# Kernel tuning notes

Hardware: AMD Instinct MI355X
Metric: run time of the kernel (lower is better)

## Reference

```python
import jax, jax.numpy as jnp
import numpy as np
from jax import lax

NUM_CLASSES = 10
NUM_ITER = 3
DN = ('NCHW', 'OIHW', 'NCHW')


def squash(t, axis=-1):
    sq = (t ** 2).sum(axis=axis, keepdims=True)
    return (sq / (1.0 + sq)) * t / jnp.sqrt(sq)


def setup_inputs() -> dict:
    key = jax.random.key(0)
    ks = jax.random.split(key, 12)
    B = 512
    s = 0.05  # param scale for numerical stability
    return {
        'x': jax.random.normal(ks[0], (B, 1, 28, 28), jnp.float32),
        'conv1_w': jax.random.normal(ks[1], (256, 1, 9, 9), jnp.float32) * s,
        'conv1_b': jax.random.normal(ks[2], (256,), jnp.float32) * s,
        'prim_w': jax.random.normal(ks[3], (8, 32, 256, 9, 9), jnp.float32) * s,
        'prim_b': jax.random.normal(ks[4], (8, 32), jnp.float32) * s,
        'route_w': jax.random.normal(ks[5], (NUM_CLASSES, 32 * 6 * 6, 8, 16), jnp.float32),
        'dec_w1': jax.random.normal(ks[6], (512, 16 * NUM_CLASSES), jnp.float32) * s,
        'dec_b1': jax.random.normal(ks[7], (512,), jnp.float32) * s,
        'dec_w2': jax.random.normal(ks[8], (1024, 512), jnp.float32) * s,
        'dec_b2': jax.random.normal(ks[9], (1024,), jnp.float32) * s,
        'dec_w3': jax.random.normal(ks[10], (784, 1024), jnp.float32) * s,
        'dec_b3': jax.random.normal(ks[11], (784,), jnp.float32) * s,
    }


def reference(x, conv1_w, conv1_b, prim_w, prim_b, route_w,
              dec_w1, dec_b1, dec_w2, dec_b2, dec_w3, dec_b3):
    B = x.shape[0]
    # conv1 + relu: [B,256,20,20]
    h = lax.conv_general_dilated(x, conv1_w, (1, 1), 'VALID', dimension_numbers=DN)
    h = jax.nn.relu(h + conv1_b[None, :, None, None])
    # primary capsules: 8 parallel convs fused into one conv with 8*32 out channels
    kw = prim_w.reshape(8 * 32, 256, 9, 9)
    u = lax.conv_general_dilated(h, kw, (2, 2), 'VALID', dimension_numbers=DN)
    u = u + prim_b.reshape(-1)[None, :, None, None]          # [B,256,6,6]
    u = u.reshape(B, 8, 32 * 6 * 6).transpose(0, 2, 1)       # [B,1152,8]
    u = squash(u, axis=-1)
    # digit capsules: priors [C,B,R,16]
    priors = jnp.einsum('bri,crio->cbro', u, route_w)
    logits = jnp.zeros_like(priors)
    for i in range(NUM_ITER):
        probs = jax.nn.softmax(logits, axis=2)
        v = squash((probs * priors).sum(axis=2, keepdims=True))  # [C,B,1,16]
        if i != NUM_ITER - 1:
            logits = logits + (priors * v).sum(axis=-1, keepdims=True)
    caps = v.squeeze(2).transpose(1, 0, 2)                    # [B,C,16]
    classes = jnp.sqrt((caps ** 2).sum(axis=-1))              # [B,C]
    classes = jax.nn.softmax(classes, axis=1)
    y = jax.nn.one_hot(jnp.argmax(classes, axis=1), NUM_CLASSES, dtype=caps.dtype)
    d = (caps * y[:, :, None]).reshape(B, -1)                 # [B,160]
    d = jax.nn.relu(d @ dec_w1.T + dec_b1)
    d = jax.nn.relu(d @ dec_w2.T + dec_b2)
    recon = jax.nn.sigmoid(d @ dec_w3.T + dec_b3)             # [B,784]
    return classes, recon
```

## Files before the change

### kernel.cpp

```cpp
#include <hip/hip_runtime.h>
#include <math.h>


typedef _Float16 f16;
typedef _Float16 f16x8 __attribute__((ext_vector_type(8)));
typedef _Float16 f16x4 __attribute__((ext_vector_type(4)));
typedef float f32x4 __attribute__((ext_vector_type(4)));

__device__ __forceinline__ void gl_lds16(const void* g, void* l) {
  __builtin_amdgcn_global_load_lds(
      (const __attribute__((address_space(1))) void*)g,
      (__attribute__((address_space(3))) void*)l, 16, 0, 0);
}

__global__ void im2col_kernel(const float* __restrict__ x, f16* __restrict__ A)
{
  const int c = blockIdx.x * 256 + threadIdx.x;
  const int m = c / 12, kc = c - m * 12;
  const int b = m / 400, rem = m - b * 400;
  const int oy = rem / 20, ox = rem - oy * 20;
  const float* xb = x + b * 784;
  f16x8 v;
#pragma unroll
  for (int j = 0; j < 8; ++j) {
    const int k = kc * 8 + j;
    float val = 0.f;
    if (k < 81) {
      const int ky = k / 9, kx = k - ky * 9;
      val = xb[(oy + ky) * 28 + ox + kx];
    }
    v[j] = (f16)val;
  }
  *(f16x8*)&A[(size_t)m * 96 + kc * 8] = v;
}

__global__ void c1trans_kernel(const float* __restrict__ w, f16* __restrict__ wt1)
{
  const int idx = blockIdx.x * 256 + threadIdx.x;
  const int oc = idx / 96, k = idx - oc * 96;
  wt1[idx] = (k < 81) ? (f16)w[oc * 81 + k] : (f16)0.f;
}

__global__ __launch_bounds__(256) void conv1_mfma_kernel(
    const f16* __restrict__ A, const f16* __restrict__ wt1,
    const float* __restrict__ bias, f16* __restrict__ ht)
{
  __shared__ f16 sm[8192];
  const int t = threadIdx.x;
  const int wv = t >> 6, lane = t & 63;
  const int id = blockIdx.x;
  const int mb = id >> 1, nb = id & 1;
  const int m0 = mb * 128, n0 = nb * 128;

  const int chunk = (lane & 3) ^ ((lane >> 3) & 3);
  long aoff[2], boff[2];
#pragma unroll
  for (int i = 0; i < 2; ++i) {
    const int r = wv * 32 + i * 16 + (lane >> 2);
    aoff[i] = (long)(m0 + r) * 192 + chunk * 16;
    boff[i] = (long)(n0 + r) * 192 + chunk * 16;
  }
  const char* ac = (const char*)A;
  const char* bc = (const char*)wt1;

  const int lrow = lane & 15, quad = lane >> 4;
  const int qx = quad ^ ((lrow >> 1) & 3);
  const int wm = wv & 1, wn = wv >> 1;
  f32x4 acc[4][4] = {};

  for (int s = 0; s < 3; ++s) {
    const long kstep = (long)s * 64;
    __syncthreads();
    {
      char* dA = (char*)sm + wv * 2048;
      char* dB = (char*)sm + 8192 + wv * 2048;
      gl_lds16(ac + aoff[0] + kstep, dA);
      gl_lds16(ac + aoff[1] + kstep, dA + 1024);
      gl_lds16(bc + boff[0] + kstep, dB);
      gl_lds16(bc + boff[1] + kstep, dB + 1024);
    }
    __syncthreads();
    const f16* As = sm;
    const f16* Bs = sm + 4096;
    f16x8 af[4], bf[4];
#pragma unroll
    for (int mt = 0; mt < 4; ++mt)
      af[mt] = *(const f16x8*)&As[(wm * 64 + mt * 16 + lrow) * 32 + qx * 8];
#pragma unroll
    for (int nt = 0; nt < 4; ++nt)
      bf[nt] = *(const f16x8*)&Bs[(wn * 64 + nt * 16 + lrow) * 32 + qx * 8];
#pragma unroll
    for (int mt = 0; mt < 4; ++mt)
#pragma unroll
      for (int nt = 0; nt < 4; ++nt)
        acc[mt][nt] = __builtin_amdgcn_mfma_f32_16x16x32_f16(
            af[mt], bf[nt], acc[mt][nt], 0, 0, 0);
  }

#pragma unroll
  for (int nt = 0; nt < 4; ++nt) {
    const int n = n0 + wn * 64 + nt * 16 + lrow;
    const float bv = bias[n];
#pragma unroll
    for (int mt = 0; mt < 4; ++mt) {
      const int mbase = m0 + wm * 64 + mt * 16 + quad * 4;
#pragma unroll
      for (int rg = 0; rg < 4; ++rg)
        ht[(size_t)(mbase + rg) * 256 + n] =
            (f16)fmaxf(acc[mt][nt][rg] + bv, 0.f);
    }
  }
}

__global__ __launch_bounds__(256) void wtrans_kernel(
    const float* __restrict__ w, f16* __restrict__ wt)
{
  __shared__ float tile[64 * 83];
  const int oc = blockIdx.x;
  const int icq = blockIdx.y;
  const int t = threadIdx.x;
  const float* src = w + (size_t)oc * 20736 + (size_t)icq * 64 * 81;
  for (int idx = t; idx < 5184; idx += 256) {
    const int ici = idx / 81, kk = idx - ici * 81;
    tile[ici * 83 + kk] = src[idx];
  }
  __syncthreads();
  f16* dst = wt + (size_t)oc * 20736 + icq * 64;
  for (int idx = t; idx < 5184; idx += 256) {
    const int kk = idx >> 6, ici = idx & 63;
    dst[kk * 256 + ici] = (f16)tile[ici * 83 + kk];
  }
}

__global__ __launch_bounds__(256) void prim_mfma_kernel(
    const f16* __restrict__ ht, const f16* __restrict__ wt,
    f16* __restrict__ part)
{
  __shared__ f16 sm[24576];
  const int t = threadIdx.x;
  const int wv = t >> 6, lane = t & 63;
  const int id = blockIdx.x;
  const int ks = (id >> 3) & 7;
  const int nb = (id >> 6) & 1;
  const int mb = (id & 7) + 8 * (id >> 7);
  const int m0 = mb * 128, n0 = nb * 128;

  const int chunk = (lane & 3) ^ ((lane >> 3) & 3);
  long aoff[2], boff[2];
#pragma unroll
  for (int i = 0; i < 2; ++i) {
    const int r = wv * 32 + i * 16 + (lane >> 2);
    const int m = m0 + r;
    const int b = m / 36, pos = m - b * 36;
    const int oy = pos / 6, ox = pos - oy * 6;
    aoff[i] = (long)(((b * 20 + 2 * oy) * 20 + 2 * ox) * 256) * 2 + chunk * 16;
    boff[i] = (long)(n0 + r) * 41472 + chunk * 16;
  }
  const char* htc = (const char*)ht;
  const char* wtc = (const char*)wt;

  const int lrow = lane & 15, quad = lane >> 4;
  const int qx = quad ^ ((lrow >> 1) & 3);
  const int wm = wv & 1, wn = wv >> 1;
  f32x4 acc[4][4] = {};

  const int s0 = ks * 81;

#define STAGE(S, BUFB)                                                        \
  {                                                                           \
    const int kykx = (S) >> 3, icb = (S) & 7;                                 \
    const int ky = kykx / 9, kx = kykx - ky * 9;                              \
    const long astep = (long)((((ky * 20 + kx) * 256) + icb * 32) * 2);       \
    const long bstep = (long)(((kykx * 256) + icb * 32) * 2);                 \
    char* dA = (char*)sm + (BUFB) + wv * 2048;                                \
    char* dB = (char*)sm + (BUFB) + 8192 + wv * 2048;                         \
    gl_lds16(htc + aoff[0] + astep, dA);                                      \
    gl_lds16(htc + aoff[1] + astep, dA + 1024);                               \
    gl_lds16(wtc + boff[0] + bstep, dB);                                      \
    gl_lds16(wtc + boff[1] + bstep, dB + 1024);                               \
  }

#define CONSUME(BUFI)                                                         \
  {                                                                           \
    const f16* As = sm + (BUFI);                                              \
    const f16* Bs = sm + (BUFI) + 4096;                                       \
    f16x8 af[4], bf[4];                                                       \
    _Pragma("unroll") for (int mt = 0; mt < 4; ++mt)                          \
        af[mt] = *(const f16x8*)&As[(wm * 64 + mt * 16 + lrow) * 32 + qx * 8];\
    _Pragma("unroll") for (int nt = 0; nt < 4; ++nt)                          \
        bf[nt] = *(const f16x8*)&Bs[(wn * 64 + nt * 16 + lrow) * 32 + qx * 8];\
    _Pragma("unroll") for (int mt = 0; mt < 4; ++mt)                          \
        _Pragma("unroll") for (int nt = 0; nt < 4; ++nt)                      \
            acc[mt][nt] = __builtin_amdgcn_mfma_f32_16x16x32_f16(             \
                af[mt], bf[nt], acc[mt][nt], 0, 0, 0);                        \
  }

  STAGE(s0, 0);
  STAGE(s0 + 1, 16384);
  int bS = 32768;
  int bC = 0;
  for (int K = 0; K < 79; ++K) {
    asm volatile("s_waitcnt vmcnt(4)" ::: "memory");
    __builtin_amdgcn_s_barrier();
    asm volatile("" ::: "memory");
    STAGE(s0 + K + 2, bS);
    __builtin_amdgcn_s_setprio(1);
    CONSUME(bC >> 1);
    __builtin_amdgcn_s_setprio(0);
    bS += 16384; if (bS == 49152) bS = 0;
    bC += 16384; if (bC == 49152) bC = 0;
  }
  asm volatile("s_waitcnt vmcnt(4)" ::: "memory");
  __builtin_amdgcn_s_barrier();
  asm volatile("" ::: "memory");
  __builtin_amdgcn_s_setprio(1);
  CONSUME(bC >> 1);
  __builtin_amdgcn_s_setprio(0);
  bC += 16384; if (bC == 49152) bC = 0;
  asm volatile("s_waitcnt vmcnt(0)" ::: "memory");
  __builtin_amdgcn_s_barrier();
  asm volatile("" ::: "memory");
  CONSUME(bC >> 1);
#undef STAGE
#undef CONSUME

  f16* pp = part + (size_t)ks * 4718592;
#pragma unroll
  for (int mt = 0; mt < 4; ++mt) {
    const int mbase = m0 + wm * 64 + mt * 16 + quad * 4;
#pragma unroll
    for (int nt = 0; nt < 4; ++nt) {
      const int n = n0 + wn * 64 + nt * 16 + lrow;
      const int np = (n & 31) * 8 + (n >> 5);
#pragma unroll
      for (int rg = 0; rg < 4; ++rg)
        pp[(size_t)(mbase + rg) * 256 + np] = (f16)acc[mt][nt][rg];
    }
  }
}

__global__ void squash_kernel(const f16* __restrict__ part,
                              const float* __restrict__ bias,
                              f16* __restrict__ u16)
{
  const int tid = blockIdx.x * 256 + threadIdx.x;
  if (tid >= 512 * 36 * 32) return;
  const int cc = tid & 31;
  const int row = tid >> 5;
  const int b = row / 36;
  const int pos = row - b * 36;
  const f16* p = part + (size_t)row * 256 + cc * 8;
  float v[8] = {};
#pragma unroll
  for (int ksl = 0; ksl < 8; ++ksl) {
    const f16x8 a = *(const f16x8*)(p + (size_t)ksl * 4718592);
#pragma unroll
    for (int i = 0; i < 8; ++i) v[i] += (float)a[i];
  }
  float sq = 0.f;
#pragma unroll
  for (int i = 0; i < 8; ++i) {
    v[i] += bias[i * 32 + cc];
    sq = fmaf(v[i], v[i], sq);
  }
  const float scale = sq / ((1.f + sq) * sqrtf(sq));
  f16x8 st;
#pragma unroll
  for (int i = 0; i < 8; ++i) st[i] = (f16)(v[i] * scale);
  *(f16x8*)&u16[(size_t)(b * 1152 + pos * 32 + cc) * 8] = st;
}

__global__ __launch_bounds__(256, 4) void priors_kernel(
    const f16* __restrict__ u16, const float* __restrict__ rw,
    f16* __restrict__ P)
{
  const int t = threadIdx.x;
  const int rl = t >> 2, oq = t & 3;
  const int rs = blockIdx.x * 64 + rl;
  const int pos = rs >> 5, cc = rs & 31;
  const int r_true = cc * 36 + pos;
  const int b0 = blockIdx.y * 64;
  const int c = blockIdx.z;

  float4 wreg[8];
  const float* wbase = rw + (size_t)(c * 1152 + r_true) * 128 + oq * 4;
#pragma unroll
  for (int k = 0; k < 8; ++k)
    wreg[k] = *(const float4*)(wbase + k * 16);

  f16* pbase = P + (size_t)((c * 512 + b0) * 1152 + rs) * 16 + oq * 4;
  const f16* ubase = u16 + (size_t)(b0 * 1152 + rs) * 8;

  for (int b = 0; b < 64; ++b) {
    const f16x8 uv = *(const f16x8*)(ubase + (size_t)b * 9216);
    float ax = 0.f, ay = 0.f, az = 0.f, aw = 0.f;
#pragma unroll
    for (int k = 0; k < 8; ++k) {
      const float uk = (float)uv[k];
      ax = fmaf(uk, wreg[k].x, ax);
      ay = fmaf(uk, wreg[k].y, ay);
      az = fmaf(uk, wreg[k].z, az);
      aw = fmaf(uk, wreg[k].w, aw);
    }
    f16x4 st;
    st[0] = (f16)ax; st[1] = (f16)ay; st[2] = (f16)az; st[3] = (f16)aw;
    *(f16x4*)(pbase + (size_t)b * 18432) = st;
  }
}

__device__ __forceinline__ float wave_sum(float v) {
#pragma unroll
  for (int off = 32; off > 0; off >>= 1) v += __shfl_xor(v, off);
  return v;
}
__device__ __forceinline__ float wave_max(float v) {
#pragma unroll
  for (int off = 32; off > 0; off >>= 1) v = fmaxf(v, __shfl_xor(v, off));
  return v;
}

__global__ __launch_bounds__(256, 2) void routing_kernel(
    const f16* __restrict__ Pg, float* __restrict__ caps)
{
  const int c = blockIdx.x >> 9;
  const int b = blockIdx.x & 511;
  const int t = threadIdx.x;
  const int wid = t >> 6;
  const int lane = t & 63;
  __shared__ float xred[4 * 17];

  float P[5][16];
  float lg[5];
  const int nk = (t < 128) ? 5 : 4;
#pragma unroll
  for (int k = 0; k < 5; ++k)
#pragma unroll
    for (int o = 0; o < 16; ++o) P[k][o] = 0.f;

  const f16* pbase = Pg + (size_t)((c * 512 + b) * 1152) * 16;
#pragma unroll
  for (int k = 0; k < 5; ++k) {
    if (k < nk) {
      const int r = t + (k << 8);
      const f16x8 p0 = *(const f16x8*)&pbase[(size_t)r * 16];
      const f16x8 p1 = *(const f16x8*)&pbase[(size_t)r * 16 + 8];
#pragma unroll
      for (int o = 0; o < 8; ++o) {
        P[k][o]     = (float)p0[o];
        P[k][o + 8] = (float)p1[o];
      }
    }
  }

  float v[16];
  {
    float sq = 0.f;
#pragma unroll
    for (int o = 0; o < 16; ++o) {
      float p = 0.f;
#pragma unroll
      for (int k = 0; k < 5; ++k) p += P[k][o];
      p = wave_sum(p);
      if (lane == 0) xred[wid * 17 + o] = p;
      v[o] = 0.f;
    }
    __syncthreads();
#pragma unroll
    for (int o = 0; o < 16; ++o) {
      const float s = (xred[o] + xred[17 + o] + xred[34 + o] + xred[51 + o]) *
                      (1.f / 1152.f);
      v[o] = s;
      sq = fmaf(s, s, sq);
    }
    const float scale = sq / ((1.f + sq) * sqrtf(sq));
#pragma unroll
    for (int o = 0; o < 16; ++o) v[o] *= scale;
    __syncthreads();
  }
#pragma unroll
  for (int k = 0; k < 5; ++k) {
    float a = 0.f;
#pragma unroll
    for (int o = 0; o < 16; ++o) a = fmaf(P[k][o], v[o], a);
    lg[k] = a;
  }

  for (int it = 1; it < 3; ++it) {
    float m = -1e30f;
#pragma unroll
    for (int k = 0; k < 5; ++k) if (k < nk) m = fmaxf(m, lg[k]);
    m = wave_max(m);
    if (lane == 0) xred[wid * 17 + 16] = m;
    __syncthreads();
    const float mx = fmaxf(fmaxf(xred[16], xred[17 + 16]),
                           fmaxf(xred[34 + 16], xred[51 + 16]));
    __syncthreads();
    float e[5];
#pragma unroll
    for (int k = 0; k < 5; ++k) e[k] = (k < nk) ? expf(lg[k] - mx) : 0.f;
    float pS = 0.f;
#pragma unroll
    for (int k = 0; k < 5; ++k) pS += e[k];
    pS = wave_sum(pS);
    if (lane == 0) xred[wid * 17 + 16] = pS;
#pragma unroll
    for (int o = 0; o < 16; ++o) {
      float p = 0.f;
#pragma unroll
      for (int k = 0; k < 5; ++k) p = fmaf(e[k], P[k][o], p);
      p = wave_sum(p);
      if (lane == 0) xred[wid * 17 + o] = p;
    }
    __syncthreads();
    const float S = xred[16] + xred[17 + 16] + xred[34 + 16] + xred[51 + 16];
    const float inv = 1.f / S;
    float sq = 0.f;
#pragma unroll
    for (int o = 0; o < 16; ++o) {
      const float s = (xred[o] + xred[17 + o] + xred[34 + o] + xred[51 + o]) * inv;
      v[o] = s;
      sq = fmaf(s, s, sq);
    }
    const float scale = sq / ((1.f + sq) * sqrtf(sq));
#pragma unroll
    for (int o = 0; o < 16; ++o) v[o] *= scale;
    __syncthreads();
    if (it < 2) {
#pragma unroll
      for (int k = 0; k < 5; ++k) {
        float a = 0.f;
#pragma unroll
        for (int o = 0; o < 16; ++o) a = fmaf(P[k][o], v[o], a);
        lg[k] += a;
      }
    }
  }
  if (t == 0) {
    float* cp = &caps[(b * 10 + c) * 16];
#pragma unroll
    for (int o = 0; o < 16; ++o) cp[o] = v[o];
  }
}

__global__ void classes_kernel(const float* __restrict__ caps,
                               float* __restrict__ out_classes,
                               float* __restrict__ d0)
{
  const int b = blockIdx.x * 256 + threadIdx.x;
  if (b >= 512) return;
  float nrm[10];
#pragma unroll
  for (int cc = 0; cc < 10; ++cc) {
    float sq = 0.f;
#pragma unroll
    for (int o = 0; o < 16; ++o) {
      const float vv = caps[(b * 10 + cc) * 16 + o];
      sq = fmaf(vv, vv, sq);
    }
    nrm[cc] = sqrtf(sq);
  }
  float mx = nrm[0]; int cs = 0;
#pragma unroll
  for (int cc = 1; cc < 10; ++cc)
    if (nrm[cc] > mx) { mx = nrm[cc]; cs = cc; }
  float e[10], ssum = 0.f;
#pragma unroll
  for (int cc = 0; cc < 10; ++cc) { e[cc] = expf(nrm[cc] - mx); ssum += e[cc]; }
  const float inv = 1.f / ssum;
#pragma unroll
  for (int cc = 0; cc < 10; ++cc) out_classes[b * 10 + cc] = e[cc] * inv;
#pragma unroll
  for (int cc = 0; cc < 10; ++cc)
#pragma unroll
    for (int o = 0; o < 16; ++o)
      d0[b * 160 + cc * 16 + o] = (cc == cs) ? caps[(b * 10 + cc) * 16 + o] : 0.f;
}

__global__ __launch_bounds__(256, 2) void fc_kernel(
    const float* __restrict__ A, const float* __restrict__ W,
    const float* __restrict__ bias, float* __restrict__ C,
    int N, int K, int act)
{
  __shared__ float As[64][17];
  __shared__ float Ws[64][17];
  const int t = threadIdx.x;
  const int tm = t >> 4, tn = t & 15;
  const int m0 = blockIdx.y << 6, n0 = blockIdx.x << 6;
  const int lr = t >> 2, lq = (t & 3) << 2;
  float acc[4][4] = {};
  for (int k0 = 0; k0 < K; k0 += 16) {
    const float4 av = *(const float4*)&A[(m0 + lr) * K + k0 + lq];
    float4 wv = make_float4(0.f, 0.f, 0.f, 0.f);
    const int wn = n0 + lr;
    if (wn < N) wv = *(const float4*)&W[wn * K + k0 + lq];
    __syncthreads();
    As[lr][lq+0] = av.x; As[lr][lq+1] = av.y; As[lr][lq+2] = av.z; As[lr][lq+3] = av.w;
    Ws[lr][lq+0] = wv.x; Ws[lr][lq+1] = wv.y; Ws[lr][lq+2] = wv.z; Ws[lr][lq+3] = wv.w;
    __syncthreads();
#pragma unroll
    for (int kk = 0; kk < 16; ++kk) {
      float a[4], w[4];
#pragma unroll
      for (int i = 0; i < 4; ++i) a[i] = As[tm * 4 + i][kk];
#pragma unroll
      for (int j = 0; j < 4; ++j) w[j] = Ws[tn * 4 + j][kk];
#pragma unroll
      for (int i = 0; i < 4; ++i)
#pragma unroll
        for (int j = 0; j < 4; ++j) acc[i][j] = fmaf(a[i], w[j], acc[i][j]);
    }
  }
#pragma unroll
  for (int i = 0; i < 4; ++i) {
    const int m = m0 + tm * 4 + i;
#pragma unroll
    for (int j = 0; j < 4; ++j) {
      const int n = n0 + tn * 4 + j;
      if (n < N) {
        float vv = acc[i][j] + bias[n];
        vv = act ? (1.f / (1.f + expf(-vv))) : fmaxf(vv, 0.f);
        C[m * N + n] = vv;
      }
    }
  }
}

extern "C" void kernel_launch(void* const* d_in, const int* in_sizes, int n_in,
                              void* d_out, int out_size, void* d_ws, size_t ws_size,
                              hipStream_t stream)
{
  const float* x       = (const float*)d_in[0];
  const float* conv1_w = (const float*)d_in[1];
  const float* conv1_b = (const float*)d_in[2];
  const float* prim_w  = (const float*)d_in[3];
  const float* prim_b  = (const float*)d_in[4];
  const float* route_w = (const float*)d_in[5];
  const float* dec_w1  = (const float*)d_in[6];
  const float* dec_b1  = (const float*)d_in[7];
  const float* dec_w2  = (const float*)d_in[8];
  const float* dec_b2  = (const float*)d_in[9];
  const float* dec_w3  = (const float*)d_in[10];
  const float* dec_b3  = (const float*)d_in[11];
  float* out = (float*)d_out;

  char* ws = (char*)d_ws;
  f16*   ht   = (f16*)(ws);
  f16*   wtp  = (f16*)(ws + 104857600);
  f16*   part = (f16*)(ws + 115474432);
  f16*   A16  = (f16*)(ws + 115474432);
  f16*   wt1  = (f16*)(ws + 190971904);
  f16*   u16  = (f16*)(ws + 191021056);
  f16*   P    = (f16*)(ws);
  float* caps = (float*)(ws + 200458240);
  float* d0   = (float*)(ws + 200785920);
  float* d1   = (float*)(ws + 201113600);
  float* d2   = (float*)(ws + 202162176);

  hipLaunchKernelGGL(im2col_kernel, dim3(9600), dim3(256), 0, stream, x, A16);
  hipLaunchKernelGGL(c1trans_kernel, dim3(96), dim3(256), 0, stream,
                     conv1_w, wt1);
  hipLaunchKernelGGL(conv1_mfma_kernel, dim3(3200), dim3(256), 0, stream,
                     A16, wt1, conv1_b, ht);
  hipLaunchKernelGGL(wtrans_kernel, dim3(256, 4), dim3(256), 0, stream,
                     prim_w, wtp);
  hipLaunchKernelGGL(prim_mfma_kernel, dim3(2304), dim3(256), 0, stream,
                     ht, wtp, part);
  hipLaunchKernelGGL(squash_kernel, dim3(2304), dim3(256), 0, stream,
                     part, prim_b, u16);
  hipLaunchKernelGGL(priors_kernel, dim3(18, 8, 10), dim3(256), 0, stream,
                     u16, route_w, P);
  hipLaunchKernelGGL(routing_kernel, dim3(5120), dim3(256), 0, stream,
                     P, caps);
  hipLaunchKernelGGL(classes_kernel, dim3(2), dim3(256), 0, stream,
                     caps, out, d0);
  hipLaunchKernelGGL(fc_kernel, dim3(8, 8), dim3(256), 0, stream,
                     d0, dec_w1, dec_b1, d1, 512, 160, 0);
  hipLaunchKernelGGL(fc_kernel, dim3(16, 8), dim3(256), 0, stream,
                     d1, dec_w2, dec_b2, d2, 1024, 512, 0);
  hipLaunchKernelGGL(fc_kernel, dim3(13, 8), dim3(256), 0, stream,
                     d2, dec_w3, dec_b3, out + 5120, 784, 1024, 1);
}
```

Measured before the change: 750.7 us.

## Fuse priors computation into routing kernel, drop materialized priors tensor

Removes the separate priors kernel that wrote a large f16 priors tensor to global memory. Each routing block now recomputes its priors from the squashed capsules and a pre-converted f16 copy of the routing weights, which a new small prep kernel produces in the capsule order used by routing. This avoids a large write and re-read of intermediate data, at the cost of extra FMAs, more registers and per-thread strided weight reads that rely on cache reuse across batch blocks.

```diff
diff --git a/kernel.cpp b/kernel.cpp
--- a/kernel.cpp
+++ b/kernel.cpp
@@ -270,42 +270,15 @@
   *(f16x8*)&u16[(size_t)(b * 1152 + pos * 32 + cc) * 8] = st;
 }
 
-__global__ __launch_bounds__(256, 4) void priors_kernel(
-    const f16* __restrict__ u16, const float* __restrict__ rw,
-    f16* __restrict__ P)
-{
-  const int t = threadIdx.x;
-  const int rl = t >> 2, oq = t & 3;
-  const int rs = blockIdx.x * 64 + rl;
+__global__ void rwprep_kernel(const float* __restrict__ rw, f16* __restrict__ rwh)
+{
+  const int rs = blockIdx.x;
+  const int c  = blockIdx.y;
+  const int t  = threadIdx.x;
   const int pos = rs >> 5, cc = rs & 31;
   const int r_true = cc * 36 + pos;
-  const int b0 = blockIdx.y * 64;
-  const int c = blockIdx.z;
-
-  float4 wreg[8];
-  const float* wbase = rw + (size_t)(c * 1152 + r_true) * 128 + oq * 4;
-#pragma unroll
-  for (int k = 0; k < 8; ++k)
-    wreg[k] = *(const float4*)(wbase + k * 16);
-
-  f16* pbase = P + (size_t)((c * 512 + b0) * 1152 + rs) * 16 + oq * 4;
-  const f16* ubase = u16 + (size_t)(b0 * 1152 + rs) * 8;
-
-  for (int b = 0; b < 64; ++b) {
-    const f16x8 uv = *(const f16x8*)(ubase + (size_t)b * 9216);
-    float ax = 0.f, ay = 0.f, az = 0.f, aw = 0.f;
-#pragma unroll
-    for (int k = 0; k < 8; ++k) {
-      const float uk = (float)uv[k];
-      ax = fmaf(uk, wreg[k].x, ax);
-      ay = fmaf(uk, wreg[k].y, ay);
-      az = fmaf(uk, wreg[k].z, az);
-      aw = fmaf(uk, wreg[k].w, aw);
-    }
-    f16x4 st;
-    st[0] = (f16)ax; st[1] = (f16)ay; st[2] = (f16)az; st[3] = (f16)aw;
-    *(f16x4*)(pbase + (size_t)b * 18432) = st;
-  }
+  const float v = rw[(size_t)(c * 1152 + r_true) * 128 + t];
+  rwh[(size_t)(c * 1152 + rs) * 128 + t] = (f16)v;
 }
 
 __device__ __forceinline__ float wave_sum(float v) {
@@ -320,7 +293,8 @@
 }
 
 __global__ __launch_bounds__(256, 2) void routing_kernel(
-    const f16* __restrict__ Pg, float* __restrict__ caps)
+    const f16* __restrict__ u16, const f16* __restrict__ rwh,
+    float* __restrict__ caps)
 {
   const int c = blockIdx.x >> 9;
   const int b = blockIdx.x & 511;
@@ -337,17 +311,26 @@
 #pragma unroll
     for (int o = 0; o < 16; ++o) P[k][o] = 0.f;
 
-  const f16* pbase = Pg + (size_t)((c * 512 + b) * 1152) * 16;
+  const f16* ub = u16 + (size_t)b * 9216;
+  const f16* wb = rwh + (size_t)c * 147456;
 #pragma unroll
   for (int k = 0; k < 5; ++k) {
     if (k < nk) {
-      const int r = t + (k << 8);
-      const f16x8 p0 = *(const f16x8*)&pbase[(size_t)r * 16];
-      const f16x8 p1 = *(const f16x8*)&pbase[(size_t)r * 16 + 8];
-#pragma unroll
-      for (int o = 0; o < 8; ++o) {
-        P[k][o]     = (float)p0[o];
-        P[k][o + 8] = (float)p1[o];
+      const int rs = t + (k << 8);
+      const f16x8 uv = *(const f16x8*)&ub[(size_t)rs * 8];
+      float uf[8];
+#pragma unroll
+      for (int i = 0; i < 8; ++i) uf[i] = (float)uv[i];
+      const f16* wr = wb + (size_t)rs * 128;
+#pragma unroll
+      for (int kk = 0; kk < 8; ++kk) {
+        const f16x8 w0 = *(const f16x8*)&wr[kk * 16];
+        const f16x8 w1 = *(const f16x8*)&wr[kk * 16 + 8];
+#pragma unroll
+        for (int o = 0; o < 8; ++o) {
+          P[k][o]     = fmaf(uf[kk], (float)w0[o], P[k][o]);
+          P[k][o + 8] = fmaf(uf[kk], (float)w1[o], P[k][o + 8]);
+        }
       }
     }
   }
@@ -550,7 +533,7 @@
   f16*   A16  = (f16*)(ws + 115474432);
   f16*   wt1  = (f16*)(ws + 190971904);
   f16*   u16  = (f16*)(ws + 191021056);
-  f16*   P    = (f16*)(ws);
+  f16*   rwh  = (f16*)(ws);
   float* caps = (float*)(ws + 200458240);
   float* d0   = (float*)(ws + 200785920);
   float* d1   = (float*)(ws + 201113600);
@@ -565,12 +548,12 @@
                      prim_w, wtp);
   hipLaunchKernelGGL(prim_mfma_kernel, dim3(2304), dim3(256), 0, stream,
                      ht, wtp, part);
+  hipLaunchKernelGGL(rwprep_kernel, dim3(1152, 10), dim3(128), 0, stream,
+                     route_w, rwh);
   hipLaunchKernelGGL(squash_kernel, dim3(2304), dim3(256), 0, stream,
                      part, prim_b, u16);
-  hipLaunchKernelGGL(priors_kernel, dim3(18, 8, 10), dim3(256), 0, stream,
-                     u16, route_w, P);
   hipLaunchKernelGGL(routing_kernel, dim3(5120), dim3(256), 0, stream,
-                     P, caps);
+                     u16, rwh, caps);
   hipLaunchKernelGGL(classes_kernel, dim3(2), dim3(256), 0, stream,
                      caps, out, d0);
   hipLaunchKernelGGL(fc_kernel, dim3(8, 8), dim3(256), 0, stream,
```

Measured after the change: 1.563 ms. +108.2%, slower.
